# Kernel optimization log

Measured on AMD Instinct MI355X. Metric: run time of the kernel, lower is better.

## Reference

```python
import jax, jax.numpy as jnp
import numpy as np

QK_I2_S = 128  # weights per block; 32 packed bytes per block
RMS_EPS = 1e-6  # RMSNorm default eps (BitNetMLP builds RMSNorm without eps arg)


def unpack_simd(packed, K):
    """Unpack SIMD block-interleaved 2-bit weights to float {-1,0,1,2}-1 values.

    packed: [M, K//4] uint8. Within each 128-weight block (32 bytes):
      byte[j] bits 6:7 -> w[j+0], 4:5 -> w[j+32], 2:3 -> w[j+64], 0:1 -> w[j+96].
    """
    M = packed.shape[0]
    nb = K // QK_I2_S
    b = packed.astype(jnp.int32).reshape(M, nb, 32)
    # stack shift groups so flattened order is [j+0..31, j+32.., j+64.., j+96..]
    w = jnp.stack([(b >> 6) & 3, (b >> 4) & 3, (b >> 2) & 3, b & 3], axis=2)  # [M,nb,4,32]
    return w.reshape(M, K).astype(jnp.float32) - 1.0


def setup_inputs() -> dict:
    key = jax.random.key(0)
    ks = jax.random.split(key, 8)
    H, I = 2560, 6912
    B, S = 4, 2048
    x = jax.random.normal(ks[0], (B, S, H), dtype=jnp.float32)
    gate_packed = jax.random.randint(ks[1], (I, H // 4), 0, 256, dtype=jnp.int32).astype(jnp.uint8)
    up_packed = jax.random.randint(ks[2], (I, H // 4), 0, 256, dtype=jnp.int32).astype(jnp.uint8)
    down_packed = jax.random.randint(ks[3], (H, I // 4), 0, 256, dtype=jnp.int32).astype(jnp.uint8)
    gate_scale = jax.random.uniform(ks[4], (1,), minval=0.01, maxval=0.1, dtype=jnp.float32)
    up_scale = jax.random.uniform(ks[5], (1,), minval=0.01, maxval=0.1, dtype=jnp.float32)
    down_scale = jax.random.uniform(ks[6], (1,), minval=0.01, maxval=0.1, dtype=jnp.float32)
    norm_w = jnp.ones((I,), dtype=jnp.float32) + 0.05 * jax.random.normal(ks[7], (I,), dtype=jnp.float32)
    return {"x": x, "gate_packed": gate_packed, "gate_scale": gate_scale,
            "up_packed": up_packed, "up_scale": up_scale,
            "down_packed": down_packed, "down_scale": down_scale,
            "norm_w": norm_w}


def reference(x, gate_packed, gate_scale, up_packed, up_scale, down_packed, down_scale, norm_w):
    H = x.shape[-1]
    I = norm_w.shape[0]
    # BitLinear (fallback path math): unpack ternary weights, apply scalar weight scale
    Wg = unpack_simd(gate_packed, H) * gate_scale[0]   # [I, H]
    Wu = unpack_simd(up_packed, H) * up_scale[0]       # [I, H]
    Wd = unpack_simd(down_packed, I) * down_scale[0]   # [H, I]
    gate = jnp.einsum('bsh,ih->bsi', x, Wg)
    up = jnp.einsum('bsh,ih->bsi', x, Wu)
    hidden = jnp.square(jax.nn.relu(gate)) * up        # ReLU^2 gating
    # RMSNorm over intermediate dim
    var = jnp.mean(jnp.square(hidden), axis=-1, keepdims=True)
    hidden = norm_w * (hidden * jax.lax.rsqrt(var + RMS_EPS))
    return jnp.einsum('bsi,hi->bsh', hidden, Wd)
```

## Files before the change

kernel.cpp:

```cpp
#include <hip/hip_runtime.h>
#include <cstdint>
#include <cstddef>

#define H_DIM 2560
#define I_DIM 6912
#define NTOK  8192

typedef __attribute__((ext_vector_type(8))) __bf16 bf16x8;
typedef __attribute__((ext_vector_type(4))) float  f32x4;

__device__ inline void gld16(void* lds, const void* g) {
    __builtin_amdgcn_global_load_lds(
        (__attribute__((address_space(1))) void*)(void*)g,
        (__attribute__((address_space(3))) void*)lds, 16, 0, 0);
}

#define NB_CVT 10240
#define NB_GU  17280
#define NB_WD  8640

__global__ __launch_bounds__(256) void prep_kernel(
    const float* __restrict__ x, __bf16* __restrict__ xb,
    const int* __restrict__ gp, const int* __restrict__ up, __bf16* __restrict__ bgu,
    const int* __restrict__ dp, const float* __restrict__ nw, __bf16* __restrict__ wdb)
{
    const int bid = blockIdx.x;
    if (bid < NB_CVT) {
        int gid = bid * 256 + threadIdx.x;
        const float4* p = (const float4*)(x + (size_t)gid * 8);
        float4 v0 = p[0], v1 = p[1];
        bf16x8 o;
        o[0] = (__bf16)v0.x; o[1] = (__bf16)v0.y; o[2] = (__bf16)v0.z; o[3] = (__bf16)v0.w;
        o[4] = (__bf16)v1.x; o[5] = (__bf16)v1.y; o[6] = (__bf16)v1.z; o[7] = (__bf16)v1.w;
        *(bf16x8*)(xb + (size_t)gid * 8) = o;
    } else if (bid < NB_CVT + NB_GU) {
        const int per_row = H_DIM >> 3;
        const int half = I_DIM * per_row;
        int gid = (bid - NB_CVT) * 256 + threadIdx.x;
        const bool isup = gid >= half;
        const int g = isup ? gid - half : gid;
        const int* packed = isup ? up : gp;
        int i  = g / per_row;
        int k0 = (g % per_row) * 8;
        int blk = k0 >> 7, grp = (k0 >> 5) & 3, j0 = k0 & 31;
        int shift = 6 - 2 * grp;
        const int* p = packed + (size_t)i * (H_DIM >> 2) + blk * 32 + j0;
        int4 v0 = *(const int4*)p;
        int4 v1 = *(const int4*)(p + 4);
        int vals[8] = {v0.x, v0.y, v0.z, v0.w, v1.x, v1.y, v1.z, v1.w};
        bf16x8 o;
#pragma unroll
        for (int b = 0; b < 8; ++b)
            o[b] = (__bf16)(float)(((vals[b] >> shift) & 3) - 1);
        int dst = (i >> 4) * 32 + (i & 15) + (isup ? 16 : 0);
        *(bf16x8*)(bgu + (size_t)dst * H_DIM + k0) = o;
    } else {
        const int per_row = I_DIM >> 3;
        int gid = (bid - NB_CVT - NB_GU) * 256 + threadIdx.x;
        int i  = gid / per_row;
        int k0 = (gid % per_row) * 8;
        int blk = k0 >> 7, grp = (k0 >> 5) & 3, j0 = k0 & 31;
        int shift = 6 - 2 * grp;
        const int* p = dp + (size_t)i * (I_DIM >> 2) + blk * 32 + j0;
        int4 v0 = *(const int4*)p;
        int4 v1 = *(const int4*)(p + 4);
        int vals[8] = {v0.x, v0.y, v0.z, v0.w, v1.x, v1.y, v1.z, v1.w};
        bf16x8 o;
#pragma unroll
        for (int b = 0; b < 8; ++b) {
            float f = (float)(((vals[b] >> shift) & 3) - 1);
            o[b] = (__bf16)(f * nw[k0 + b]);
        }
        *(bf16x8*)(wdb + (size_t)i * I_DIM + k0) = o;
    }
}

template<int KDIM>
__global__ __launch_bounds__(512, 2) void gemm_gu8(
    const __bf16* __restrict__ A,
    const __bf16* __restrict__ B,
    const float* __restrict__ gs_p,
    const float* __restrict__ us_p,
    __bf16* __restrict__ hidden,
    float* rsbuf,
    int nby)
{
    constexpr int KB = KDIM * 2;
    constexpr int NT = KDIM / 64;
    __shared__ __align__(16) char smem[131072];

    const int nwg = (int)gridDim.x;
    const int q = nwg >> 3;
    const int id = (int)blockIdx.x;
    const int wg = (id & 7) * q + (id >> 3);
    const int bx = wg / nby, by = wg % nby;
    const int m0 = bx * 256, n0 = by * 256;

    const int t = (int)threadIdx.x;
    const int lane = t & 63;
    const int wid = t >> 6;
    const int wm = wid >> 2, wn = wid & 3;
    const int l15 = lane & 15, s8 = lane >> 4;

    const int qa  = (t & 7) ^ ((t >> 3) & 7);
    const int rA2 = ((t >> 3) << 1) + (qa >> 2);
    const char* gA0 = (const char*)A + (size_t)(m0 + rA2) * KB + (qa & 3) * 16;
    const char* gA1 = (const char*)A + (size_t)(m0 + 128 + rA2) * KB + (qa & 3) * 16;
    const int sr0 = t >> 3, sr1 = 64 + (t >> 3);
    const int br0 = ((sr0 >> 5) << 6) + (sr0 & 31);
    const int br1 = ((sr1 >> 5) << 6) + (sr1 & 31);
    const char* gB0 = (const char*)B + (size_t)(n0 + br0) * KB + qa * 16;
    const char* gB1 = (const char*)B + (size_t)(n0 + br1) * KB + qa * 16;
    char* ldst = smem + t * 16;

    const int aoff = (wm * 64 + (l15 >> 1)) * 128 +
                     (((((l15 & 1) << 2) | s8) ^ ((l15 >> 1) & 7)) << 4);
    const int boff = (wn * 32 + l15) * 128;
    const int bco0 = ((s8) ^ (l15 & 7)) << 4;
    const int bco1 = ((4 | s8) ^ (l15 & 7)) << 4;

    f32x4 acc[8][4];
#pragma unroll
    for (int f = 0; f < 8; ++f)
#pragma unroll
        for (int n = 0; n < 4; ++n) acc[f][n] = (f32x4){0, 0, 0, 0};

#define STG_A(d, kt, kk) do {                                              \
        size_t _oA = (size_t)(kt) * 128 + (kk) * 64;                       \
        gld16(ldst + (d) * 65536 + (kk) * 16384,        gA0 + _oA);        \
        gld16(ldst + (d) * 65536 + (kk) * 16384 + 8192, gA1 + _oA);        \
    } while (0)
#define STG_B(d, kt, nh) do {                                              \
        size_t _oB = (size_t)(nh) * 32 * KB + (size_t)(kt) * 128;          \
        gld16(ldst + (d) * 65536 + 32768 + (nh) * 16384,        gB0 + _oB);\
        gld16(ldst + (d) * 65536 + 32768 + (nh) * 16384 + 8192, gB1 + _oB);\
    } while (0)
#define LOAD_A(d, kk) do { _Pragma("unroll")                               \
        for (int _f = 0; _f < 8; ++_f)                                     \
            a[_f] = *(const bf16x8*)(smem + (d) * 65536 + (kk) * 16384 +   \
                                     _f * 1024 + aoff); } while (0)
#define LOAD_B(d, nh) do {                                                 \
        b0 = *(const bf16x8*)(smem + (d) * 65536 + 32768 + (nh) * 16384 +  \
                              boff + bcur);                                \
        b1 = *(const bf16x8*)(smem + (d) * 65536 + 32768 + (nh) * 16384 +  \
                              boff + bcur + 2048); } while (0)
#define MFMA16(nh) do { __builtin_amdgcn_s_setprio(1); _Pragma("unroll")   \
        for (int _f = 0; _f < 8; ++_f) {                                   \
            acc[_f][(nh) * 2] = __builtin_amdgcn_mfma_f32_16x16x32_bf16(   \
                a[_f], b0, acc[_f][(nh) * 2], 0, 0, 0);                    \
            acc[_f][(nh) * 2 + 1] = __builtin_amdgcn_mfma_f32_16x16x32_bf16(\
                a[_f], b1, acc[_f][(nh) * 2 + 1], 0, 0, 0); }              \
        __builtin_amdgcn_s_setprio(0); } while (0)
#define BAR() do { asm volatile("" ::: "memory");                          \
        __builtin_amdgcn_s_barrier();                                      \
        asm volatile("" ::: "memory"); } while (0)
#define WAITK() do { asm volatile("s_waitcnt lgkmcnt(0)" ::: "memory");    \
        __builtin_amdgcn_sched_barrier(0); } while (0)

    STG_A(0, 0, 0); STG_A(0, 0, 1); STG_B(0, 0, 0); STG_B(0, 0, 1);
    STG_A(1, 1, 0); STG_B(1, 1, 0);
    asm volatile("s_waitcnt vmcnt(4)" ::: "memory");
    BAR();

    bf16x8 a[8], b0, b1;
    for (int kt = 0; kt < NT; ++kt) {
        const int d = kt & 1;
        int bcur = bco0;
        LOAD_A(d, 0); LOAD_B(d, 0);
        if (kt + 1 < NT) STG_A(d ^ 1, kt + 1, 1);
        WAITK(); MFMA16(0); BAR();
        LOAD_B(d, 1);
        if (kt + 1 < NT) STG_B(d ^ 1, kt + 1, 1);
        WAITK(); MFMA16(1); BAR();
        bcur = bco1;
        LOAD_A(d, 1); LOAD_B(d, 0);
        if (kt + 2 < NT) STG_A(d, kt + 2, 0);
        WAITK(); MFMA16(0); BAR();
        LOAD_B(d, 1);
        if (kt + 2 < NT) {
            STG_B(d, kt + 2, 0);
            asm volatile("s_waitcnt vmcnt(4)" ::: "memory");
        } else {
            asm volatile("s_waitcnt vmcnt(0)" ::: "memory");
        }
        WAITK(); MFMA16(1); BAR();
    }

#undef STG_A
#undef STG_B
#undef LOAD_A
#undef LOAD_B
#undef MFMA16
#undef BAR
#undef WAITK

    const float comb = gs_p[0] * gs_p[0] * us_p[0];
    const int r0 = m0 + wm * 128 + s8 * 4;
#pragma unroll
    for (int f = 0; f < 8; ++f)
#pragma unroll
        for (int j = 0; j < 4; ++j) {
            float ssum = 0.f;
#pragma unroll
            for (int p = 0; p < 2; ++p) {
                float g = acc[f][2 * p][j];
                float u = acc[f][2 * p + 1][j];
                float r = fmaxf(g, 0.f);
                float h = comb * r * r * u;
                hidden[(size_t)(r0 + f * 16 + j) * I_DIM +
                       ((by * 8 + wn * 2 + p) * 16 + l15)] = (__bf16)h;
                ssum += h * h;
            }
            ssum += __shfl_xor(ssum, 1, 64);
            ssum += __shfl_xor(ssum, 2, 64);
            ssum += __shfl_xor(ssum, 4, 64);
            ssum += __shfl_xor(ssum, 8, 64);
            if (l15 == 0) atomicAdd(&rsbuf[r0 + f * 16 + j], ssum);
        }
}

template<int KDIM>
__global__ __launch_bounds__(512) void gemm_down_pipe(
    const __bf16* __restrict__ A,
    const __bf16* __restrict__ B,
    const float* __restrict__ ds_p,
    const float* __restrict__ rs,
    float* __restrict__ outf,
    int nby)
{
    constexpr int BM = 256, BN = 128, BK = 64;
    constexpr int NT = KDIM / BK;
    constexpr int SLOTB = (BM + BN) * BK * 2;
    __shared__ __align__(16) char smem[3 * SLOTB];

    const int nwg = (int)gridDim.x;
    const int q = nwg >> 3;
    const int id = (int)blockIdx.x;
    const int wg = (id & 7) * q + (id >> 3);
    const int bx = wg / nby;
    const int by = wg % nby;

    const int m0 = bx * BM;
    const int n0 = by * BN;
    const int t  = (int)threadIdx.x;
    const int lane = t & 63;
    const int wm = (t >> 6) >> 1;
    const int wn = (t >> 6) & 1;

    const int srow = t >> 3;
    const int scol = ((t & 7) * 16) ^ ((srow & 7) << 4);
    const char* gA = (const char*)A + (size_t)(m0 + srow) * (KDIM * 2) + scol;
    const char* gB = (const char*)B + (size_t)(n0 + srow) * (KDIM * 2) + scol;
    char* lbase = smem + t * 16;

    const int l15 = lane & 15;
    const int xv  = (l15 & 7) << 4;
    const int colx[2] = { (((lane >> 4) * 16) ^ xv), ((64 + (lane >> 4) * 16) ^ xv) };

    f32x4 acc[4][4];
#pragma unroll
    for (int a = 0; a < 4; ++a)
#pragma unroll
        for (int b = 0; b < 4; ++b) acc[a][b] = (f32x4){0, 0, 0, 0};

#define STAGE_T(s, kt) do {                                                     \
        char* _ls = lbase + (s) * SLOTB;                                        \
        const char* _ga = gA + (kt) * (BK * 2);                                 \
        _Pragma("unroll")                                                       \
        for (int _i = 0; _i < 4; ++_i)                                          \
            gld16(_ls + _i * 8192, _ga + (size_t)_i * 64 * (KDIM * 2));         \
        const char* _gb = gB + (kt) * (BK * 2);                                 \
        char* _lb = _ls + BM * BK * 2;                                          \
        _Pragma("unroll")                                                       \
        for (int _i = 0; _i < 2; ++_i)                                          \
            gld16(_lb + _i * 8192, _gb + (size_t)_i * 64 * (KDIM * 2));         \
    } while (0)

#define COMPUTE_T(s) do {                                                       \
        const char* _sa = smem + (s) * SLOTB;                                   \
        const char* _sb = _sa + BM * BK * 2;                                    \
        _Pragma("unroll")                                                       \
        for (int _kk = 0; _kk < 2; ++_kk) {                                     \
            bf16x8 _a[4], _b[4];                                                \
            _Pragma("unroll")                                                   \
            for (int _f = 0; _f < 4; ++_f)                                      \
                _a[_f] = *(const bf16x8*)(_sa + (wm * 64 + _f * 16 + l15) * 128 + colx[_kk]); \
            _Pragma("unroll")                                                   \
            for (int _f = 0; _f < 4; ++_f)                                      \
                _b[_f] = *(const bf16x8*)(_sb + (wn * 64 + _f * 16 + l15) * 128 + colx[_kk]); \
            __builtin_amdgcn_s_setprio(1);                                      \
            _Pragma("unroll")                                                   \
            for (int _fm = 0; _fm < 4; ++_fm)                                   \
                _Pragma("unroll")                                               \
                for (int _fn = 0; _fn < 4; ++_fn)                               \
                    acc[_fm][_fn] = __builtin_amdgcn_mfma_f32_16x16x32_bf16(    \
                        _a[_fm], _b[_fn], acc[_fm][_fn], 0, 0, 0);              \
            __builtin_amdgcn_s_setprio(0);                                      \
        }                                                                       \
    } while (0)

    STAGE_T(0, 0);
    STAGE_T(1, 1);
    asm volatile("s_waitcnt vmcnt(6)" ::: "memory");
    __builtin_amdgcn_s_barrier();
    asm volatile("" ::: "memory");

    for (int kt = 0; kt < NT; ++kt) {
        if (kt + 2 < NT) STAGE_T((kt + 2) % 3, kt + 2);
        COMPUTE_T(kt % 3);
        if (kt + 2 < NT) {
            asm volatile("s_waitcnt vmcnt(6)" ::: "memory");
            __builtin_amdgcn_s_barrier();
            asm volatile("" ::: "memory");
        } else if (kt + 2 == NT) {
            asm volatile("s_waitcnt vmcnt(0)" ::: "memory");
            __builtin_amdgcn_s_barrier();
            asm volatile("" ::: "memory");
        }
    }

#undef STAGE_T
#undef COMPUTE_T

    const float ds = ds_p[0];
    const int r0 = m0 + wm * 64 + (lane >> 4) * 4;
#pragma unroll
    for (int fm = 0; fm < 4; ++fm)
#pragma unroll
        for (int j = 0; j < 4; ++j) {
            const int row = r0 + fm * 16 + j;
            const float sc = ds * rsqrtf(rs[row] * (1.f / I_DIM) + 1e-6f);
#pragma unroll
            for (int fn = 0; fn < 4; ++fn)
                outf[(size_t)row * H_DIM + (n0 + wn * 64 + fn * 16 + l15)] =
                    sc * acc[fm][fn][j];
        }
}

extern "C" void kernel_launch(void* const* d_in, const int* in_sizes, int n_in,
                              void* d_out, int out_size, void* d_ws, size_t ws_size,
                              hipStream_t stream) {
    const float* x   = (const float*)d_in[0];
    const int*   gp  = (const int*)d_in[1];
    const float* gs  = (const float*)d_in[2];
    const int*   upk = (const int*)d_in[3];
    const float* us  = (const float*)d_in[4];
    const int*   dp  = (const int*)d_in[5];
    const float* dsc = (const float*)d_in[6];
    const float* nw  = (const float*)d_in[7];
    float* out = (float*)d_out;

    char* ws = (char*)d_ws;
    __bf16* xb     = (__bf16*)ws;  ws += (size_t)NTOK * H_DIM * 2;
    __bf16* bgu    = (__bf16*)ws;  ws += (size_t)2 * I_DIM * H_DIM * 2;
    __bf16* wdb    = (__bf16*)ws;  ws += (size_t)H_DIM * I_DIM * 2;
    __bf16* hidden = (__bf16*)ws;  ws += (size_t)NTOK * I_DIM * 2;
    float*  rsbuf  = (float*)ws;   ws += (size_t)NTOK * 4;

    hipMemsetAsync(rsbuf, 0, (size_t)NTOK * 4, stream);

    prep_kernel<<<NB_CVT + NB_GU + NB_WD, 256, 0, stream>>>(
        x, xb, gp, upk, bgu, dp, nw, wdb);

    gemm_gu8<H_DIM><<<dim3((NTOK / 256) * (2 * I_DIM / 256)), 512, 0, stream>>>(
        xb, bgu, gs, us, hidden, rsbuf, 2 * I_DIM / 256);

    gemm_down_pipe<I_DIM><<<dim3((NTOK / 256) * (H_DIM / 128)), 512, 0, stream>>>(
        hidden, wdb, dsc, rsbuf, out, H_DIM / 128);
}
```

Before: 857.0 us.

## Move RMS sum-of-squares to separate kernel, add barriers, widen down-GEMM N tile

Drops the per-tile atomicAdd sum-of-squares reduction from the gate/up GEMM epilogue. A new kernel re-reads the bf16 hidden tensor and writes the per-row rsqrt, so the memset goes away and the down GEMM epilogue becomes a plain multiply. The down GEMM N tile grows from 128 to 160, giving 5 MFMA columns per wave and fewer workgroups. An extra barrier is also added before each MFMA phase in the gate/up loop. The cost is an extra ~113MB read of hidden, extra syncs, and higher register/LDS pressure in the down GEMM. The norm now uses the bf16-rounded hidden values rather than fp32.

```diff
diff --git a/kernel.cpp b/kernel.cpp
--- a/kernel.cpp
+++ b/kernel.cpp
@@ -75,6 +75,27 @@
     }
 }
 
+__global__ __launch_bounds__(256) void rms_rs_kernel(const __bf16* __restrict__ hidden,
+                                                     float* __restrict__ rs) {
+    const int tk = blockIdx.x;
+    const __bf16* row = hidden + (size_t)tk * I_DIM;
+    float s = 0.f;
+    for (int idx = threadIdx.x; idx < I_DIM / 8; idx += 256) {
+        bf16x8 v = *(const bf16x8*)&row[idx * 8];
+#pragma unroll
+        for (int j = 0; j < 8; ++j) { float f = (float)v[j]; s += f * f; }
+    }
+#pragma unroll
+    for (int off = 32; off; off >>= 1) s += __shfl_down(s, off, 64);
+    __shared__ float wsum[4];
+    if ((threadIdx.x & 63) == 0) wsum[threadIdx.x >> 6] = s;
+    __syncthreads();
+    if (threadIdx.x == 0) {
+        float tot = wsum[0] + wsum[1] + wsum[2] + wsum[3];
+        rs[tk] = rsqrtf(tot / (float)I_DIM + 1e-6f);
+    }
+}
+
 template<int KDIM>
 __global__ __launch_bounds__(512, 2) void gemm_gu8(
     const __bf16* __restrict__ A,
@@ -82,7 +103,6 @@
     const float* __restrict__ gs_p,
     const float* __restrict__ us_p,
     __bf16* __restrict__ hidden,
-    float* rsbuf,
     int nby)
 {
     constexpr int KB = KDIM * 2;
@@ -168,14 +188,14 @@
         int bcur = bco0;
         LOAD_A(d, 0); LOAD_B(d, 0);
         if (kt + 1 < NT) STG_A(d ^ 1, kt + 1, 1);
-        WAITK(); MFMA16(0); BAR();
+        BAR(); WAITK(); MFMA16(0); BAR();
         LOAD_B(d, 1);
         if (kt + 1 < NT) STG_B(d ^ 1, kt + 1, 1);
-        WAITK(); MFMA16(1); BAR();
+        BAR(); WAITK(); MFMA16(1); BAR();
         bcur = bco1;
         LOAD_A(d, 1); LOAD_B(d, 0);
         if (kt + 2 < NT) STG_A(d, kt + 2, 0);
-        WAITK(); MFMA16(0); BAR();
+        BAR(); WAITK(); MFMA16(0); BAR();
         LOAD_B(d, 1);
         if (kt + 2 < NT) {
             STG_B(d, kt + 2, 0);
@@ -183,7 +203,7 @@
         } else {
             asm volatile("s_waitcnt vmcnt(0)" ::: "memory");
         }
-        WAITK(); MFMA16(1); BAR();
+        BAR(); WAITK(); MFMA16(1); BAR();
     }
 
 #undef STG_A
@@ -199,24 +219,15 @@
 #pragma unroll
     for (int f = 0; f < 8; ++f)
 #pragma unroll
-        for (int j = 0; j < 4; ++j) {
-            float ssum = 0.f;
-#pragma unroll
-            for (int p = 0; p < 2; ++p) {
+        for (int p = 0; p < 2; ++p)
+#pragma unroll
+            for (int j = 0; j < 4; ++j) {
                 float g = acc[f][2 * p][j];
                 float u = acc[f][2 * p + 1][j];
                 float r = fmaxf(g, 0.f);
-                float h = comb * r * r * u;
                 hidden[(size_t)(r0 + f * 16 + j) * I_DIM +
-                       ((by * 8 + wn * 2 + p) * 16 + l15)] = (__bf16)h;
-                ssum += h * h;
+                       ((by * 8 + wn * 2 + p) * 16 + l15)] = (__bf16)(comb * r * r * u);
             }
-            ssum += __shfl_xor(ssum, 1, 64);
-            ssum += __shfl_xor(ssum, 2, 64);
-            ssum += __shfl_xor(ssum, 4, 64);
-            ssum += __shfl_xor(ssum, 8, 64);
-            if (l15 == 0) atomicAdd(&rsbuf[r0 + f * 16 + j], ssum);
-        }
 }
 
 template<int KDIM>
@@ -228,7 +239,7 @@
     float* __restrict__ outf,
     int nby)
 {
-    constexpr int BM = 256, BN = 128, BK = 64;
+    constexpr int BM = 256, BN = 160, BK = 64;
     constexpr int NT = KDIM / BK;
     constexpr int SLOTB = (BM + BN) * BK * 2;
     __shared__ __align__(16) char smem[3 * SLOTB];
@@ -257,11 +268,11 @@
     const int xv  = (l15 & 7) << 4;
     const int colx[2] = { (((lane >> 4) * 16) ^ xv), ((64 + (lane >> 4) * 16) ^ xv) };
 
-    f32x4 acc[4][4];
+    f32x4 acc[4][5];
 #pragma unroll
     for (int a = 0; a < 4; ++a)
 #pragma unroll
-        for (int b = 0; b < 4; ++b) acc[a][b] = (f32x4){0, 0, 0, 0};
+        for (int b = 0; b < 5; ++b) acc[a][b] = (f32x4){0, 0, 0, 0};
 
 #define STAGE_T(s, kt) do {                                                     \
         char* _ls = lbase + (s) * SLOTB;                                        \
@@ -274,6 +285,8 @@
         _Pragma("unroll")                                                       \
         for (int _i = 0; _i < 2; ++_i)                                          \
             gld16(_lb + _i * 8192, _gb + (size_t)_i * 64 * (KDIM * 2));         \
+        if (t < 256)                                                            \
+            gld16(_lb + 2 * 8192, _gb + (size_t)2 * 64 * (KDIM * 2));           \
     } while (0)
 
 #define COMPUTE_T(s) do {                                                       \
@@ -281,18 +294,18 @@
         const char* _sb = _sa + BM * BK * 2;                                    \
         _Pragma("unroll")                                                       \
         for (int _kk = 0; _kk < 2; ++_kk) {                                     \
-            bf16x8 _a[4], _b[4];                                                \
+            bf16x8 _a[4], _b[5];                                                \
             _Pragma("unroll")                                                   \
             for (int _f = 0; _f < 4; ++_f)                                      \
                 _a[_f] = *(const bf16x8*)(_sa + (wm * 64 + _f * 16 + l15) * 128 + colx[_kk]); \
             _Pragma("unroll")                                                   \
-            for (int _f = 0; _f < 4; ++_f)                                      \
-                _b[_f] = *(const bf16x8*)(_sb + (wn * 64 + _f * 16 + l15) * 128 + colx[_kk]); \
+            for (int _f = 0; _f < 5; ++_f)                                      \
+                _b[_f] = *(const bf16x8*)(_sb + (wn * 80 + _f * 16 + l15) * 128 + colx[_kk]); \
             __builtin_amdgcn_s_setprio(1);                                      \
             _Pragma("unroll")                                                   \
             for (int _fm = 0; _fm < 4; ++_fm)                                   \
                 _Pragma("unroll")                                               \
-                for (int _fn = 0; _fn < 4; ++_fn)                               \
+                for (int _fn = 0; _fn < 5; ++_fn)                               \
                     acc[_fm][_fn] = __builtin_amdgcn_mfma_f32_16x16x32_bf16(    \
                         _a[_fm], _b[_fn], acc[_fm][_fn], 0, 0, 0);              \
             __builtin_amdgcn_s_setprio(0);                                      \
@@ -329,10 +342,10 @@
 #pragma unroll
         for (int j = 0; j < 4; ++j) {
             const int row = r0 + fm * 16 + j;
-            const float sc = ds * rsqrtf(rs[row] * (1.f / I_DIM) + 1e-6f);
-#pragma unroll
-            for (int fn = 0; fn < 4; ++fn)
-                outf[(size_t)row * H_DIM + (n0 + wn * 64 + fn * 16 + l15)] =
+            const float sc = ds * rs[row];
+#pragma unroll
+            for (int fn = 0; fn < 5; ++fn)
+                outf[(size_t)row * H_DIM + (n0 + wn * 80 + fn * 16 + l15)] =
                     sc * acc[fm][fn][j];
         }
 }
@@ -357,14 +370,14 @@
     __bf16* hidden = (__bf16*)ws;  ws += (size_t)NTOK * I_DIM * 2;
     float*  rsbuf  = (float*)ws;   ws += (size_t)NTOK * 4;
 
-    hipMemsetAsync(rsbuf, 0, (size_t)NTOK * 4, stream);
-
     prep_kernel<<<NB_CVT + NB_GU + NB_WD, 256, 0, stream>>>(
         x, xb, gp, upk, bgu, dp, nw, wdb);
 
     gemm_gu8<H_DIM><<<dim3((NTOK / 256) * (2 * I_DIM / 256)), 512, 0, stream>>>(
-        xb, bgu, gs, us, hidden, rsbuf, 2 * I_DIM / 256);
-
-    gemm_down_pipe<I_DIM><<<dim3((NTOK / 256) * (H_DIM / 128)), 512, 0, stream>>>(
-        hidden, wdb, dsc, rsbuf, out, H_DIM / 128);
-}
+        xb, bgu, gs, us, hidden, 2 * I_DIM / 256);
+
+    rms_rs_kernel<<<NTOK, 256, 0, stream>>>(hidden, rsbuf);
+
+    gemm_down_pipe<I_DIM><<<dim3((NTOK / 256) * (H_DIM / 160)), 512, 0, stream>>>(
+        hidden, wdb, dsc, rsbuf, out, H_DIM / 160);
+}
```

After: 769.0 us. 1.11x faster.
